# Performance work log

Measured on AMD Instinct MI355X. Metric: run time of the kernel, lower is better.

The kernel has to match this reference:

```python
import jax, jax.numpy as jnp
import numpy as np

B, L, F = 16, 1024, 64
D = 256          # d_model (expand_factor=1 -> d_inner == d_model)
S = 2            # num_scales
N = 16           # state_size
H = 32           # fc hidden
EPS = 1e-5


def setup_inputs() -> dict:
    key = jax.random.key(0)
    ks = jax.random.split(key, 20)
    g = lambda i, shape, s=0.05: jax.random.normal(ks[i], shape, dtype=jnp.float32) * s
    return {
        "x": jax.random.normal(ks[0], (B, L, F), dtype=jnp.float32),
        "W_in": g(1, (F, D)), "b_in": jnp.zeros((D,), jnp.float32),
        # per-scale liquid-Mamba params, stacked over scales
        "Wd": g(2, (S, D, D)), "bd": jnp.zeros((S, D), jnp.float32),
        "WB": g(3, (S, D, N)), "WC": g(4, (S, D, N)),
        "Wtau": g(5, (S, D, D)),
        "A_log": jnp.broadcast_to(jnp.log(jnp.arange(1, N + 1, dtype=jnp.float32)), (S, D, N)).copy(),
        "Dp": jnp.ones((S, D), jnp.float32),
        "Wout": g(6, (S, D, D)),
        # head
        "ln_g": jnp.ones((D,), jnp.float32), "ln_b": jnp.zeros((D,), jnp.float32),
        "W1": g(7, (D, H)), "b1": jnp.zeros((H,), jnp.float32),
        "W2": g(8, (H, 1)), "b2": jnp.zeros((1,), jnp.float32),
    }


def _liquid_ssm(x, Wd, bd, WB, WC, Wtau, A_log, Dp, Wout):
    # x: [B,L,D] -> y: [B,L,D]. Selective scan with liquid time-constant gate.
    delta = jax.nn.softplus(jnp.einsum('bld,de->ble', x, Wd) + bd)   # [B,L,D]
    tau = jax.nn.sigmoid(jnp.einsum('bld,de->ble', x, Wtau))          # liquid gate
    delta = delta * tau
    Bm = jnp.einsum('bld,dn->bln', x, WB)                             # [B,L,N]
    Cm = jnp.einsum('bld,dn->bln', x, WC)                             # [B,L,N]
    A = -jnp.exp(A_log)                                               # [D,N]
    dA = jnp.exp(delta[..., None] * A)                                # [B,L,D,N]
    dBx = delta[..., None] * Bm[:, :, None, :] * x[..., None]         # [B,L,D,N]

    def step(h, inp):
        a_t, bx_t, c_t = inp                                          # [B,D,N],[B,D,N],[B,N]
        h = a_t * h + bx_t
        y = jnp.einsum('bdn,bn->bd', h, c_t)
        return h, y

    h0 = jnp.zeros((x.shape[0], x.shape[2], A.shape[1]), x.dtype)
    _, ys = jax.lax.scan(step, h0,
                         (dA.transpose(1, 0, 2, 3), dBx.transpose(1, 0, 2, 3), Cm.transpose(1, 0, 2)))
    y = ys.transpose(1, 0, 2) + x * Dp                                # skip connection
    return jnp.einsum('bld,de->ble', y, Wout)


def reference(x, W_in, b_in, Wd, bd, WB, WC, Wtau, A_log, Dp, Wout,
              ln_g, ln_b, W1, b1, W2, b2):
    h = jnp.einsum('blf,fd->bld', x, W_in) + b_in                     # input projection
    outs = [_liquid_ssm(h, Wd[s], bd[s], WB[s], WC[s], Wtau[s], A_log[s], Dp[s], Wout[s])
            for s in range(Wd.shape[0])]
    mamba_out = sum(outs) / len(outs)                                 # average over scales
    last = mamba_out[:, -1, :]                                        # [B,D]
    mu = jnp.mean(last, axis=-1, keepdims=True)
    var = jnp.var(last, axis=-1, keepdims=True)
    z = (last - mu) * jax.lax.rsqrt(var + EPS) * ln_g + ln_b          # LayerNorm
    z = jax.nn.relu(z @ W1 + b1)                                      # dropout is identity in eval
    return z @ W2 + b2                                                # [B,1]
```

## Files before the change

kernel.cpp:

```cpp
#include <hip/hip_runtime.h>
#include <hip/hip_bf16.h>
#include <math.h>

#define B_   16
#define L_   1024
#define F_   64
#define D_   256
#define S_   2
#define N_   16
#define H_   32
#define EPS_ 1e-5f
#define BL_  (B_*L_)
#define NCH_ 4
#define TC_  (L_/NCH_)
#define SUB_ 64
#define TSTR_ 68
#define LOG2E_ 1.44269504088896340736f

typedef __attribute__((ext_vector_type(8))) short  bf16x8;
typedef __attribute__((ext_vector_type(4))) float  f32x4;
typedef __attribute__((ext_vector_type(2))) float  f32x2;

typedef const __attribute__((address_space(1))) void* gas_ptr;
typedef __attribute__((address_space(3))) void*       las_ptr;

#if defined(__has_builtin)
# if __has_builtin(__builtin_amdgcn_exp2f)
#  define EXP2(x) __builtin_amdgcn_exp2f(x)
#  define ASCALE_ LOG2E_
# endif
#endif
#ifndef EXP2
# define EXP2(x) __expf(x)
# define ASCALE_ 1.0f
#endif

__device__ inline void async_copy16(const void* g, void* l) {
    __builtin_amdgcn_global_load_lds((gas_ptr)g, (las_ptr)l, 16, 0, 0);
}

__device__ inline unsigned short f2bf_rne(float x) {
    union { float f; unsigned u; } v; v.f = x;
    unsigned r = v.u + 0x7fff + ((v.u >> 16) & 1);
    return (unsigned short)(r >> 16);
}
__device__ inline float bf2f(unsigned short h) {
    union { float f; unsigned u; } v; v.u = ((unsigned)h) << 16;
    return v.f;
}

__global__ __launch_bounds__(256) void k_xsplit(const float* __restrict__ x,
                                                unsigned short* __restrict__ xh,
                                                unsigned short* __restrict__ xl)
{
    const int i = (blockIdx.x * 256 + threadIdx.x) * 4;
    float4 v = *(const float4*)(x + i);
    ushort4 h4, l4;
    unsigned short hh;
    hh = f2bf_rne(v.x); h4.x = hh; l4.x = f2bf_rne(v.x - bf2f(hh));
    hh = f2bf_rne(v.y); h4.y = hh; l4.y = f2bf_rne(v.y - bf2f(hh));
    hh = f2bf_rne(v.z); h4.z = hh; l4.z = f2bf_rne(v.z - bf2f(hh));
    hh = f2bf_rne(v.w); h4.w = hh; l4.w = f2bf_rne(v.w - bf2f(hh));
    *(ushort4*)(xh + i) = h4;
    *(ushort4*)(xl + i) = l4;
}

__global__ __launch_bounds__(64) void k_prep_w(const float* __restrict__ Win,
                                               const float* __restrict__ bin,
                                               const float* __restrict__ Wd,
                                               const float* __restrict__ bd,
                                               const float* __restrict__ Wt,
                                               const float* __restrict__ WB,
                                               unsigned short* __restrict__ Weff_hi,
                                               unsigned short* __restrict__ Weff_lo,
                                               float* __restrict__ bias_eff,
                                               unsigned short* __restrict__ WinT_hi,
                                               unsigned short* __restrict__ WinT_lo,
                                               unsigned short* __restrict__ WBe_hi,
                                               unsigned short* __restrict__ WBe_lo,
                                               float* __restrict__ bbias)
{
    const int i = blockIdx.x;
    const int f = threadIdx.x;
    __shared__ float col[D_];

    if (i < S_ * 512) {
        const int s = i >> 9, n = i & 511;
        const float* W = (n < 256) ? (Wd + (size_t)s * D_ * D_) : (Wt + (size_t)s * D_ * D_);
        const int e = n & 255;
        for (int d = f; d < D_; d += 64) col[d] = W[(size_t)d * D_ + e];
        __syncthreads();
        float a = 0.f;
        for (int d = 0; d < D_; ++d) a += Win[(size_t)f * D_ + d] * col[d];
        unsigned short hi = f2bf_rne(a);
        size_t o = ((size_t)s * 512 + n) * F_ + f;
        Weff_hi[o] = hi;
        Weff_lo[o] = f2bf_rne(a - bf2f(hi));
        if (f == 0) {
            float bb = 0.f;
            for (int d = 0; d < D_; ++d) bb += bin[d] * col[d];
            if (n < 256) bb += bd[s * D_ + e];
            bias_eff[s * 512 + n] = bb;
        }
    } else if (i < S_ * 512 + D_) {
        const int d = i - S_ * 512;
        float v = Win[(size_t)f * D_ + d];
        unsigned short hi = f2bf_rne(v);
        size_t o = (size_t)d * F_ + f;
        WinT_hi[o] = hi;
        WinT_lo[o] = f2bf_rne(v - bf2f(hi));
    } else {
        const int idx = i - (S_ * 512 + D_);
        const int s = idx >> 4, n = idx & 15;
        const float* wb = WB + (size_t)s * D_ * N_;
        float a = 0.f;
        for (int d = 0; d < D_; ++d) a += Win[(size_t)f * D_ + d] * wb[(size_t)d * N_ + n];
        unsigned short hi = f2bf_rne(a);
        size_t o = ((size_t)s * N_ + n) * F_ + f;
        WBe_hi[o] = hi;
        WBe_lo[o] = f2bf_rne(a - bf2f(hi));
        if (f == 0) {
            float bb = 0.f;
            for (int d = 0; d < D_; ++d) bb += bin[d] * wb[(size_t)d * N_ + n];
            bbias[s * N_ + n] = bb;
        }
    }
}

__global__ __launch_bounds__(256) void k_fused_scan(
        const unsigned short* __restrict__ x_hi,
        const unsigned short* __restrict__ x_lo,
        const unsigned short* __restrict__ Weff_hi,
        const unsigned short* __restrict__ Weff_lo,
        const unsigned short* __restrict__ WinT_hi,
        const unsigned short* __restrict__ WinT_lo,
        const unsigned short* __restrict__ WBe_hi,
        const unsigned short* __restrict__ WBe_lo,
        const float* __restrict__ bias_eff,
        const float* __restrict__ bin,
        const float* __restrict__ bbias,
        const float* __restrict__ A_log,
        float* __restrict__ part,
        float* __restrict__ csum)
{
    const int dtile = blockIdx.x >> 2;
    const int c     = blockIdx.x & 3;
    const int b     = blockIdx.y;
    const int s     = blockIdx.z;
    const int d0    = dtile * 16;
    const int tid   = threadIdx.x;
    const int wid   = tid >> 6;
    const int lane  = tid & 63;
    const int l15   = lane & 15;
    const int quad  = lane >> 4;
    const int dl    = tid & 15;
    const int nl    = tid >> 4;

    __shared__ unsigned short Wh[64 * F_];
    __shared__ unsigned short Wl[64 * F_];
    __shared__ float sdl[16][TSTR_];
    __shared__ float sq [16][TSTR_];
    __shared__ float sb [16][TSTR_];

    const int r8 = lane >> 3;
    const int c8 = lane & 7;

    #pragma unroll
    for (int call = 0; call < 2; ++call) {
        const int rr = call * 8 + r8;
        const int ar = wid * 16 + rr;
        const int lc = (c8 - ar) & 7;
        const unsigned short *gh, *gl;
        if (wid == 0)      { size_t o = ((size_t)s * 512 + d0 + rr) * F_ + lc * 8;       gh = Weff_hi + o; gl = Weff_lo + o; }
        else if (wid == 1) { size_t o = ((size_t)s * 512 + 256 + d0 + rr) * F_ + lc * 8; gh = Weff_hi + o; gl = Weff_lo + o; }
        else if (wid == 2) { size_t o = ((size_t)(d0 + rr)) * F_ + lc * 8;               gh = WinT_hi + o; gl = WinT_lo + o; }
        else               { size_t o = ((size_t)s * N_ + rr) * F_ + lc * 8;             gh = WBe_hi + o;  gl = WBe_lo + o; }
        async_copy16(gh, &Wh[(wid * 16 + call * 8) * F_]);
        async_copy16(gl, &Wl[(wid * 16 + call * 8) * F_]);
    }

    const float bias_d = bias_eff[s * 512 + d0 + l15];
    const float bias_t = bias_eff[s * 512 + 256 + d0 + l15];
    const float bin_v  = bin[d0 + l15];
    const float bb_v   = bbias[s * N_ + l15];
    const float A2 = -__expf(A_log[((size_t)s * D_ + d0 + dl) * N_ + nl]) * ASCALE_;

    f32x2 st01 = {0.f, 0.f};
    f32x2 st23 = {0.f, 0.f};
    float As = 0.f;

    const int qoff = quad * 8;
    const int nsc  = TC_ / SUB_;

    bf16x8 fah0, fah1, fal0, fal1;
    {
        const size_t rowb = ((size_t)b * L_ + c * TC_ + (nsc - 1) * SUB_ + wid * 16 + l15) * F_;
        fah0 = *(const bf16x8*)(x_hi + rowb + qoff);
        fah1 = *(const bf16x8*)(x_hi + rowb + 32 + qoff);
        fal0 = *(const bf16x8*)(x_lo + rowb + qoff);
        fal1 = *(const bf16x8*)(x_lo + rowb + 32 + qoff);
    }
    __syncthreads();

    for (int sc = nsc - 1; sc >= 0; --sc) {
        f32x4 acc[4];
        #pragma unroll
        for (int g = 0; g < 4; ++g) acc[g] = (f32x4){0.f, 0.f, 0.f, 0.f};
        #pragma unroll
        for (int ks = 0; ks < 2; ++ks) {
            bf16x8 ah = ks ? fah1 : fah0;
            bf16x8 al = ks ? fal1 : fal0;
            #pragma unroll
            for (int g = 0; g < 4; ++g) {
                const int brow = g * 16 + l15;
                const int pcB  = ((ks * 4 + quad) + brow) & 7;
                bf16x8 bh = *(const bf16x8*)&Wh[brow * F_ + pcB * 8];
                bf16x8 bl = *(const bf16x8*)&Wl[brow * F_ + pcB * 8];
                acc[g] = __builtin_amdgcn_mfma_f32_16x16x32_bf16(ah, bh, acc[g], 0, 0, 0);
                acc[g] = __builtin_amdgcn_mfma_f32_16x16x32_bf16(ah, bl, acc[g], 0, 0, 0);
                acc[g] = __builtin_amdgcn_mfma_f32_16x16x32_bf16(al, bh, acc[g], 0, 0, 0);
            }
        }

        bf16x8 nah0, nah1, nal0, nal1;
        const bool more = (sc > 0);
        if (more) {
            const size_t rowb = ((size_t)b * L_ + c * TC_ + (sc - 1) * SUB_ + wid * 16 + l15) * F_;
            nah0 = *(const bf16x8*)(x_hi + rowb + qoff);
            nah1 = *(const bf16x8*)(x_hi + rowb + 32 + qoff);
            nal0 = *(const bf16x8*)(x_lo + rowb + qoff);
            nal1 = *(const bf16x8*)(x_lo + rowb + 32 + qoff);
        }

        __syncthreads();

        {
            f32x4 wd_, wq_, wb_;
            #pragma unroll
            for (int r = 0; r < 4; ++r) {
                const float pd  = acc[0][r] + bias_d;
                const float sp  = fmaxf(pd, 0.f) + __logf(1.f + __expf(-fabsf(pd)));
                const float sg  = 1.f / (1.f + __expf(-(acc[1][r] + bias_t)));
                const float dlt = sp * sg;
                const float hv  = acc[2][r] + bin_v;
                wd_[r] = dlt;
                wq_[r] = dlt * hv;
                wb_[r] = acc[3][r] + bb_v;
            }
            const int tcol = wid * 16 + quad * 4;
            *(f32x4*)&sdl[l15][tcol] = wd_;
            *(f32x4*)&sq [l15][tcol] = wq_;
            *(f32x4*)&sb [l15][tcol] = wb_;
        }
        __syncthreads();

        #pragma unroll 4
        for (int tt = SUB_ - 4; tt >= 0; tt -= 4) {
            f32x4 dp = *(const f32x4*)&sdl[dl][tt];
            f32x4 qp = *(const f32x4*)&sq [dl][tt];
            f32x4 bp = *(const f32x4*)&sb [nl][tt];
            const float a2v = fmaf(A2, dp.w, As);
            const float a1v = fmaf(A2, dp.z, a2v);
            const float a0v = fmaf(A2, dp.y, a1v);
            f32x2 e01, e23;
            e23.y = EXP2(As);
            e23.x = EXP2(a2v);
            e01.y = EXP2(a1v);
            e01.x = EXP2(a0v);
            f32x2 q01 = {qp.x, qp.y}, q23 = {qp.z, qp.w};
            f32x2 b01 = {bp.x, bp.y}, b23 = {bp.z, bp.w};
            st01 = q01 * b01 * e01 + st01;
            st23 = q23 * b23 * e23 + st23;
            As = fmaf(A2, dp.x, a0v);
        }

        if (more) { fah0 = nah0; fah1 = nah1; fal0 = nal0; fal1 = nal1; }
    }

    const size_t pb = ((size_t)s * B_ + b) * NCH_ + c;
    part[(pb * D_ + d0 + dl) * N_ + nl] = (st01.x + st01.y) + (st23.x + st23.y);
    if (nl == 0)
        csum[pb * D_ + d0 + dl] = As / A2;
}

__global__ __launch_bounds__(256) void k_scan_comb(const float* __restrict__ part,
                                                   const float* __restrict__ csum,
                                                   const float* __restrict__ A_log,
                                                   float* __restrict__ states)
{
    const int b   = blockIdx.y;
    const int s   = blockIdx.z;
    const int tid = threadIdx.x;
    const int dl  = tid & 15;
    const int nl  = tid >> 4;
    const int d   = blockIdx.x * 16 + dl;

    const float A = -__expf(A_log[((size_t)s * D_ + d) * N_ + nl]);

    const size_t cbase = ((size_t)s * B_ + b) * NCH_;
    float cs[NCH_];
    #pragma unroll
    for (int c = 0; c < NCH_; ++c) cs[c] = csum[(cbase + c) * D_ + d];

    float state = 0.f;
    float tail = 0.f;
    #pragma unroll
    for (int c = NCH_ - 1; c >= 0; --c) {
        float p = part[((cbase + c) * D_ + d) * N_ + nl];
        state += __expf(A * tail) * p;
        tail  += cs[c];
    }
    states[(((size_t)s * B_ + b) * D_ + d) * N_ + nl] = state;
}

__global__ __launch_bounds__(256) void k_final(const float* __restrict__ x,
                                               const float* __restrict__ Win,
                                               const float* __restrict__ bin,
                                               const float* __restrict__ states,
                                               const float* __restrict__ WC,
                                               const float* __restrict__ Dp,
                                               const float* __restrict__ Wout,
                                               const float* __restrict__ ln_g,
                                               const float* __restrict__ ln_b,
                                               const float* __restrict__ W1,
                                               const float* __restrict__ b1,
                                               const float* __restrict__ W2,
                                               const float* __restrict__ b2,
                                               float* __restrict__ out)
{
    const int b   = blockIdx.x;
    const int tid = threadIdx.x;

    __shared__ float xr[F_];
    __shared__ float hl[D_];
    __shared__ float cm[S_][N_];
    __shared__ float ys[S_][D_];
    __shared__ float zv[D_];
    __shared__ float red1[256];
    __shared__ float red2[256];
    __shared__ float r1[H_];

    if (tid < F_) xr[tid] = x[((size_t)b * L_ + (L_ - 1)) * F_ + tid];
    __syncthreads();

    {
        float a = bin[tid];
        for (int f = 0; f < F_; ++f) a += xr[f] * Win[(size_t)f * D_ + tid];
        hl[tid] = a;
    }
    __syncthreads();

    if (tid < S_ * N_) {
        int s = tid >> 4, n = tid & 15;
        float a = 0.f;
        for (int d = 0; d < D_; ++d) a += hl[d] * WC[((size_t)s * D_ + d) * N_ + n];
        cm[s][n] = a;
    }
    __syncthreads();

    for (int s = 0; s < S_; ++s) {
        const float* st = states + (((size_t)s * B_ + b) * D_ + tid) * N_;
        float a = 0.f;
        #pragma unroll
        for (int n = 0; n < N_; ++n) a += st[n] * cm[s][n];
        ys[s][tid] = a + hl[tid] * Dp[s * D_ + tid];
    }
    __syncthreads();

    float v;
    {
        float a = 0.f;
        for (int s = 0; s < S_; ++s) {
            const float* wo = Wout + (size_t)s * D_ * D_;
            for (int d = 0; d < D_; ++d) a += ys[s][d] * wo[(size_t)d * D_ + tid];
        }
        v = a * (1.f / S_);
    }

    red1[tid] = v;
    red2[tid] = v * v;
    __syncthreads();
    for (int off = 128; off > 0; off >>= 1) {
        if (tid < off) { red1[tid] += red1[tid + off]; red2[tid] += red2[tid + off]; }
        __syncthreads();
    }
    const float mu  = red1[0] * (1.f / D_);
    const float var = red2[0] * (1.f / D_) - mu * mu;
    const float z = (v - mu) * rsqrtf(var + EPS_) * ln_g[tid] + ln_b[tid];
    zv[tid] = z;
    __syncthreads();

    if (tid < H_) {
        float a = b1[tid];
        for (int e = 0; e < D_; ++e) a += zv[e] * W1[(size_t)e * H_ + tid];
        r1[tid] = fmaxf(a, 0.f);
    }
    __syncthreads();
    if (tid == 0) {
        float a = b2[0];
        for (int j = 0; j < H_; ++j) a += r1[j] * W2[j];
        out[b] = a;
    }
}

extern "C" void kernel_launch(void* const* d_in, const int* in_sizes, int n_in,
                              void* d_out, int out_size, void* d_ws, size_t ws_size,
                              hipStream_t stream)
{
    const float* x     = (const float*)d_in[0];
    const float* Win   = (const float*)d_in[1];
    const float* bin   = (const float*)d_in[2];
    const float* Wd    = (const float*)d_in[3];
    const float* bd    = (const float*)d_in[4];
    const float* WB    = (const float*)d_in[5];
    const float* WC    = (const float*)d_in[6];
    const float* Wtau  = (const float*)d_in[7];
    const float* A_log = (const float*)d_in[8];
    const float* Dp    = (const float*)d_in[9];
    const float* Wout  = (const float*)d_in[10];
    const float* ln_g  = (const float*)d_in[11];
    const float* ln_b  = (const float*)d_in[12];
    const float* W1    = (const float*)d_in[13];
    const float* b1    = (const float*)d_in[14];
    const float* W2    = (const float*)d_in[15];
    const float* b2    = (const float*)d_in[16];
    float* out = (float*)d_out;

    char* ws = (char*)d_ws;
    const size_t MB = 1024 * 1024;
    const size_t KB = 1024;
    unsigned short* x_hi     = (unsigned short*)(ws);
    unsigned short* x_lo     = (unsigned short*)(ws + 2 * MB);
    unsigned short* Weff_hi  = (unsigned short*)(ws + 4 * MB);
    unsigned short* Weff_lo  = (unsigned short*)(ws + 4 * MB + 128 * KB);
    unsigned short* WinT_hi  = (unsigned short*)(ws + 4 * MB + 256 * KB);
    unsigned short* WinT_lo  = (unsigned short*)(ws + 4 * MB + 288 * KB);
    unsigned short* WBe_hi   = (unsigned short*)(ws + 4 * MB + 320 * KB);
    unsigned short* WBe_lo   = (unsigned short*)(ws + 4 * MB + 324 * KB);
    float*          bias_eff = (float*)(ws + 4 * MB + 328 * KB);
    float*          bbias    = (float*)(ws + 4 * MB + 332 * KB);
    float*          part     = (float*)(ws + 5 * MB);
    float*          csum     = (float*)(ws + 7 * MB);
    float*          states   = (float*)(ws + 8 * MB);

    hipLaunchKernelGGL(k_xsplit,    dim3(BL_ * F_ / 1024),        dim3(256), 0, stream, x, x_hi, x_lo);
    hipLaunchKernelGGL(k_prep_w,    dim3(S_ * 512 + D_ + S_ * N_),dim3(64),  0, stream,
                       Win, bin, Wd, bd, Wtau, WB,
                       Weff_hi, Weff_lo, bias_eff, WinT_hi, WinT_lo, WBe_hi, WBe_lo, bbias);
    hipLaunchKernelGGL(k_fused_scan, dim3((D_ / 16) * NCH_, B_, S_), dim3(256), 0, stream,
                       x_hi, x_lo, Weff_hi, Weff_lo, WinT_hi, WinT_lo, WBe_hi, WBe_lo,
                       bias_eff, bin, bbias, A_log, part, csum);
    hipLaunchKernelGGL(k_scan_comb, dim3(D_ / 16, B_, S_),        dim3(256), 0, stream, part, csum, A_log, states);
    hipLaunchKernelGGL(k_final,     dim3(B_),                     dim3(256), 0, stream,
                       x, Win, bin, states, WC, Dp, Wout, ln_g, ln_b, W1, b1, W2, b2, out);
}
```

Baseline: 175.9 us.

## Merge prep kernels, double scan chunks, fold chunk combine into final kernel

Folds the x bf16 split and weight-precompute kernels into one launch, packing four weight jobs per 256-thread block. Splits the sequence into eight chunks instead of four, doubling the scan grid for more parallelism. Removes the separate chunk-combine kernel by evaluating the chunk carries inside the final head kernel, contracting with C directly. The final kernel now does more per-thread exp work over 8x16 partials, and the larger part buffer pushes csum to a new workspace offset.

```diff
diff --git a/kernel.cpp b/kernel.cpp
--- a/kernel.cpp
+++ b/kernel.cpp
@@ -11,11 +11,12 @@
 #define H_   32
 #define EPS_ 1e-5f
 #define BL_  (B_*L_)
-#define NCH_ 4
+#define NCH_ 8
 #define TC_  (L_/NCH_)
 #define SUB_ 64
 #define TSTR_ 68
 #define LOG2E_ 1.44269504088896340736f
+#define XBLK_ (BL_*F_/1024)
 
 typedef __attribute__((ext_vector_type(8))) short  bf16x8;
 typedef __attribute__((ext_vector_type(4))) float  f32x4;
@@ -49,68 +50,75 @@
     return v.f;
 }
 
-__global__ __launch_bounds__(256) void k_xsplit(const float* __restrict__ x,
-                                                unsigned short* __restrict__ xh,
-                                                unsigned short* __restrict__ xl)
+__global__ __launch_bounds__(256) void k_prep(const float* __restrict__ x,
+                                              const float* __restrict__ Win,
+                                              const float* __restrict__ bin,
+                                              const float* __restrict__ Wd,
+                                              const float* __restrict__ bd,
+                                              const float* __restrict__ Wt,
+                                              const float* __restrict__ WB,
+                                              unsigned short* __restrict__ x_hi,
+                                              unsigned short* __restrict__ x_lo,
+                                              unsigned short* __restrict__ Weff_hi,
+                                              unsigned short* __restrict__ Weff_lo,
+                                              float* __restrict__ bias_eff,
+                                              unsigned short* __restrict__ WinT_hi,
+                                              unsigned short* __restrict__ WinT_lo,
+                                              unsigned short* __restrict__ WBe_hi,
+                                              unsigned short* __restrict__ WBe_lo,
+                                              float* __restrict__ bbias)
 {
-    const int i = (blockIdx.x * 256 + threadIdx.x) * 4;
-    float4 v = *(const float4*)(x + i);
-    ushort4 h4, l4;
-    unsigned short hh;
-    hh = f2bf_rne(v.x); h4.x = hh; l4.x = f2bf_rne(v.x - bf2f(hh));
-    hh = f2bf_rne(v.y); h4.y = hh; l4.y = f2bf_rne(v.y - bf2f(hh));
-    hh = f2bf_rne(v.z); h4.z = hh; l4.z = f2bf_rne(v.z - bf2f(hh));
-    hh = f2bf_rne(v.w); h4.w = hh; l4.w = f2bf_rne(v.w - bf2f(hh));
-    *(ushort4*)(xh + i) = h4;
-    *(ushort4*)(xl + i) = l4;
-}
-
-__global__ __launch_bounds__(64) void k_prep_w(const float* __restrict__ Win,
-                                               const float* __restrict__ bin,
-                                               const float* __restrict__ Wd,
-                                               const float* __restrict__ bd,
-                                               const float* __restrict__ Wt,
-                                               const float* __restrict__ WB,
-                                               unsigned short* __restrict__ Weff_hi,
-                                               unsigned short* __restrict__ Weff_lo,
-                                               float* __restrict__ bias_eff,
-                                               unsigned short* __restrict__ WinT_hi,
-                                               unsigned short* __restrict__ WinT_lo,
-                                               unsigned short* __restrict__ WBe_hi,
-                                               unsigned short* __restrict__ WBe_lo,
-                                               float* __restrict__ bbias)
-{
-    const int i = blockIdx.x;
-    const int f = threadIdx.x;
-    __shared__ float col[D_];
-
-    if (i < S_ * 512) {
-        const int s = i >> 9, n = i & 511;
+    const int blk = blockIdx.x;
+    const int tid = threadIdx.x;
+
+    if (blk < XBLK_) {
+        const int i = (blk * 256 + tid) * 4;
+        float4 v = *(const float4*)(x + i);
+        ushort4 h4, l4;
+        unsigned short hh;
+        hh = f2bf_rne(v.x); h4.x = hh; l4.x = f2bf_rne(v.x - bf2f(hh));
+        hh = f2bf_rne(v.y); h4.y = hh; l4.y = f2bf_rne(v.y - bf2f(hh));
+        hh = f2bf_rne(v.z); h4.z = hh; l4.z = f2bf_rne(v.z - bf2f(hh));
+        hh = f2bf_rne(v.w); h4.w = hh; l4.w = f2bf_rne(v.w - bf2f(hh));
+        *(ushort4*)(x_hi + i) = h4;
+        *(ushort4*)(x_lo + i) = l4;
+        return;
+    }
+
+    const int job4 = blk - XBLK_;
+    const int j    = tid >> 6;
+    const int f    = tid & 63;
+    const int job  = job4 * 4 + j;
+
+    __shared__ float col[4][D_];
+
+    if (job < 1024) {
+        const int s = job >> 9, n = job & 511;
         const float* W = (n < 256) ? (Wd + (size_t)s * D_ * D_) : (Wt + (size_t)s * D_ * D_);
         const int e = n & 255;
-        for (int d = f; d < D_; d += 64) col[d] = W[(size_t)d * D_ + e];
+        for (int d = f; d < D_; d += 64) col[j][d] = W[(size_t)d * D_ + e];
         __syncthreads();
         float a = 0.f;
-        for (int d = 0; d < D_; ++d) a += Win[(size_t)f * D_ + d] * col[d];
+        for (int d = 0; d < D_; ++d) a += Win[(size_t)f * D_ + d] * col[j][d];
         unsigned short hi = f2bf_rne(a);
         size_t o = ((size_t)s * 512 + n) * F_ + f;
         Weff_hi[o] = hi;
         Weff_lo[o] = f2bf_rne(a - bf2f(hi));
         if (f == 0) {
             float bb = 0.f;
-            for (int d = 0; d < D_; ++d) bb += bin[d] * col[d];
+            for (int d = 0; d < D_; ++d) bb += bin[d] * col[j][d];
             if (n < 256) bb += bd[s * D_ + e];
             bias_eff[s * 512 + n] = bb;
         }
-    } else if (i < S_ * 512 + D_) {
-        const int d = i - S_ * 512;
+    } else if (job < 1024 + D_) {
+        const int d = job - 1024;
         float v = Win[(size_t)f * D_ + d];
         unsigned short hi = f2bf_rne(v);
         size_t o = (size_t)d * F_ + f;
         WinT_hi[o] = hi;
         WinT_lo[o] = f2bf_rne(v - bf2f(hi));
     } else {
-        const int idx = i - (S_ * 512 + D_);
+        const int idx = job - (1024 + D_);
         const int s = idx >> 4, n = idx & 15;
         const float* wb = WB + (size_t)s * D_ * N_;
         float a = 0.f;
@@ -143,8 +151,8 @@
         float* __restrict__ part,
         float* __restrict__ csum)
 {
-    const int dtile = blockIdx.x >> 2;
-    const int c     = blockIdx.x & 3;
+    const int dtile = blockIdx.x >> 3;
+    const int c     = blockIdx.x & 7;
     const int b     = blockIdx.y;
     const int s     = blockIdx.z;
     const int d0    = dtile * 16;
@@ -283,40 +291,12 @@
         csum[pb * D_ + d0 + dl] = As / A2;
 }
 
-__global__ __launch_bounds__(256) void k_scan_comb(const float* __restrict__ part,
-                                                   const float* __restrict__ csum,
-                                                   const float* __restrict__ A_log,
-                                                   float* __restrict__ states)
-{
-    const int b   = blockIdx.y;
-    const int s   = blockIdx.z;
-    const int tid = threadIdx.x;
-    const int dl  = tid & 15;
-    const int nl  = tid >> 4;
-    const int d   = blockIdx.x * 16 + dl;
-
-    const float A = -__expf(A_log[((size_t)s * D_ + d) * N_ + nl]);
-
-    const size_t cbase = ((size_t)s * B_ + b) * NCH_;
-    float cs[NCH_];
-    #pragma unroll
-    for (int c = 0; c < NCH_; ++c) cs[c] = csum[(cbase + c) * D_ + d];
-
-    float state = 0.f;
-    float tail = 0.f;
-    #pragma unroll
-    for (int c = NCH_ - 1; c >= 0; --c) {
-        float p = part[((cbase + c) * D_ + d) * N_ + nl];
-        state += __expf(A * tail) * p;
-        tail  += cs[c];
-    }
-    states[(((size_t)s * B_ + b) * D_ + d) * N_ + nl] = state;
-}
-
 __global__ __launch_bounds__(256) void k_final(const float* __restrict__ x,
                                                const float* __restrict__ Win,
                                                const float* __restrict__ bin,
-                                               const float* __restrict__ states,
+                                               const float* __restrict__ part,
+                                               const float* __restrict__ csum,
+                                               const float* __restrict__ A_log,
                                                const float* __restrict__ WC,
                                                const float* __restrict__ Dp,
                                                const float* __restrict__ Wout,
@@ -359,11 +339,25 @@
     __syncthreads();
 
     for (int s = 0; s < S_; ++s) {
-        const float* st = states + (((size_t)s * B_ + b) * D_ + tid) * N_;
-        float a = 0.f;
+        const float* al = A_log + ((size_t)s * D_ + tid) * N_;
+        float a2v[N_];
         #pragma unroll
-        for (int n = 0; n < N_; ++n) a += st[n] * cm[s][n];
-        ys[s][tid] = a + hl[tid] * Dp[s * D_ + tid];
+        for (int n = 0; n < N_; ++n) a2v[n] = -__expf(al[n]);
+        const size_t cbase = ((size_t)s * B_ + b) * NCH_;
+        float cs[NCH_];
+        #pragma unroll
+        for (int c = 0; c < NCH_; ++c) cs[c] = csum[(cbase + c) * D_ + tid];
+        float acc = 0.f;
+        float tail = 0.f;
+        #pragma unroll
+        for (int c = NCH_ - 1; c >= 0; --c) {
+            const float* pp = part + ((cbase + c) * D_ + tid) * N_;
+            #pragma unroll
+            for (int n = 0; n < N_; ++n)
+                acc += cm[s][n] * __expf(a2v[n] * tail) * pp[n];
+            tail += cs[c];
+        }
+        ys[s][tid] = acc + hl[tid] * Dp[s * D_ + tid];
     }
     __syncthreads();
 
@@ -440,17 +434,16 @@
     float*          bias_eff = (float*)(ws + 4 * MB + 328 * KB);
     float*          bbias    = (float*)(ws + 4 * MB + 332 * KB);
     float*          part     = (float*)(ws + 5 * MB);
-    float*          csum     = (float*)(ws + 7 * MB);
-    float*          states   = (float*)(ws + 8 * MB);
-
-    hipLaunchKernelGGL(k_xsplit,    dim3(BL_ * F_ / 1024),        dim3(256), 0, stream, x, x_hi, x_lo);
-    hipLaunchKernelGGL(k_prep_w,    dim3(S_ * 512 + D_ + S_ * N_),dim3(64),  0, stream,
-                       Win, bin, Wd, bd, Wtau, WB,
-                       Weff_hi, Weff_lo, bias_eff, WinT_hi, WinT_lo, WBe_hi, WBe_lo, bbias);
+    float*          csum     = (float*)(ws + 9 * MB);
+
+    hipLaunchKernelGGL(k_prep, dim3(XBLK_ + 328), dim3(256), 0, stream,
+                       x, Win, bin, Wd, bd, Wtau, WB,
+                       x_hi, x_lo, Weff_hi, Weff_lo, bias_eff,
+                       WinT_hi, WinT_lo, WBe_hi, WBe_lo, bbias);
     hipLaunchKernelGGL(k_fused_scan, dim3((D_ / 16) * NCH_, B_, S_), dim3(256), 0, stream,
                        x_hi, x_lo, Weff_hi, Weff_lo, WinT_hi, WinT_lo, WBe_hi, WBe_lo,
                        bias_eff, bin, bbias, A_log, part, csum);
-    hipLaunchKernelGGL(k_scan_comb, dim3(D_ / 16, B_, S_),        dim3(256), 0, stream, part, csum, A_log, states);
-    hipLaunchKernelGGL(k_final,     dim3(B_),                     dim3(256), 0, stream,
-                       x, Win, bin, states, WC, Dp, Wout, ln_g, ln_b, W1, b1, W2, b2, out);
-}
+    hipLaunchKernelGGL(k_final, dim3(B_), dim3(256), 0, stream,
+                       x, Win, bin, part, csum, A_log, WC, Dp, Wout,
+                       ln_g, ln_b, W1, b1, W2, b2, out);
+}
```

Measured after the change: 187.9 us. +6.8%, slower.
